# Kernel tuning notes

Measured on AMD Instinct MI355X. Metric: run time of the kernel, lower is better.

Reference implementation:

```python
import jax, jax.numpy as jnp
import numpy as np

N_NODES = 100000
N_EDGES = 1600000
IN_DIM = 128
HID2 = 128   # hidden_dim * 2
OUT_DIM = 1


def setup_inputs() -> dict:
    key = jax.random.key(0)
    ks = jax.random.split(key, 9)
    x = jax.random.normal(ks[0], (N_NODES, IN_DIM), dtype=jnp.float32)
    edge_index = jax.random.randint(ks[1], (2, N_EDGES), 0, N_NODES, dtype=jnp.int32)
    s_in = 1.0 / np.sqrt(IN_DIM)
    s_h = 1.0 / np.sqrt(HID2)
    W_conv = jax.random.normal(ks[2], (IN_DIM, HID2), dtype=jnp.float32) * s_in
    b_conv = jnp.zeros((HID2,), dtype=jnp.float32)
    W_proj = jax.random.normal(ks[3], (IN_DIM, HID2), dtype=jnp.float32) * s_in
    b_proj = jax.random.normal(ks[4], (HID2,), dtype=jnp.float32) * s_in
    W_out = jax.random.normal(ks[5], (HID2, OUT_DIM), dtype=jnp.float32) * s_h
    b_out = jax.random.normal(ks[6], (OUT_DIM,), dtype=jnp.float32) * s_h
    return {"x": x, "edge_index": edge_index, "W_conv": W_conv, "b_conv": b_conv,
            "W_proj": W_proj, "b_proj": b_proj, "W_out": W_out, "b_out": b_out}


def reference(x, edge_index, W_conv, b_conv, W_proj, b_proj, W_out, b_out):
    n = x.shape[0]
    loops = jnp.arange(n, dtype=edge_index.dtype)
    self_loops = jnp.stack([loops, loops])  # [2, N]
    # self loops added twice: once in forward() explicitly, once inside GCNConv (default)
    ei = jnp.concatenate([edge_index, self_loops, self_loops], axis=1)
    row, col = ei[0], ei[1]  # source -> destination
    # symmetric GCN normalization: deg computed over destinations
    deg = jax.ops.segment_sum(jnp.ones_like(row, dtype=x.dtype), col, num_segments=n)
    dinv = jnp.where(deg > 0, deg ** -0.5, 0.0)
    norm = dinv[row] * dinv[col]  # [E']
    xw = x @ W_conv  # [N, HID2]
    msgs = xw[row] * norm[:, None]  # [E', HID2] gather + scale
    conv = jax.ops.segment_sum(msgs, col, num_segments=n) + b_conv
    combined = jax.nn.relu(conv + x @ W_proj + b_proj)
    out = combined @ W_out + b_out  # [N, 1]
    return out.squeeze()
```

## Files before the change

### kernel.cpp

```cpp
#include <hip/hip_runtime.h>

#define N_NODES 100000
#define N_EDGES 1600000
#define DIM 128
#define NBIN 128
#define WINSZ 782
#define SLOT 64
#define CH 4096
#define NP1 ((N_EDGES + CH - 1) / CH)
#define SUBCAP 80
#define NGEMM ((N_NODES + 63) / 64)
#define SENT 0xFFFFFFFFu

typedef __attribute__((ext_vector_type(8))) short short8;
typedef __attribute__((ext_vector_type(4))) float f32x4;

__device__ inline unsigned short bf16u(float f) {
    unsigned u = __builtin_bit_cast(unsigned, f);
    return (unsigned short)((u + 0x7FFFu + ((u >> 16) & 1u)) >> 16);
}
__device__ inline unsigned pk_bf16(float a, float b) {
    return (unsigned)bf16u(a) | ((unsigned)bf16u(b) << 16);
}
__device__ inline float bf16_lo(unsigned v) { return __builtin_bit_cast(float, v << 16); }
__device__ inline float bf16_hi(unsigned v) { return __builtin_bit_cast(float, v & 0xFFFF0000u); }

__device__ inline unsigned pk_fp8x4(float a, float b, float c, float d) {
    int lo = __builtin_amdgcn_cvt_pk_fp8_f32(a, b, 0, false);
    int hi = __builtin_amdgcn_cvt_pk_fp8_f32(c, d, lo, true);
    return (unsigned)hi;
}
__device__ inline float fp8_b0(int v) { return __builtin_amdgcn_cvt_f32_fp8(v, 0); }
__device__ inline float fp8_b1(int v) { return __builtin_amdgcn_cvt_f32_fp8(v, 1); }


__launch_bounds__(256)
__global__ void k_prep(const float* __restrict__ Wc, const float* __restrict__ Wp,
                       const int* __restrict__ erow, const int* __restrict__ ecol,
                       int* __restrict__ cntT, unsigned* __restrict__ gbin,
                       unsigned short* __restrict__ WtG) {
    const int tid = threadIdx.x;
    if (blockIdx.x >= NP1) {
        int idx = (blockIdx.x - NP1) * 256 + tid;
        int n = idx >> 7, k = idx & 127;
        float v = (n < 128) ? Wc[k * 128 + n] : Wp[k * 128 + (n - 128)];
        int t = n >> 4, mm = n & 15;
        int q = k >> 5, qd = (k >> 3) & 3, j = k & 7;
        WtG[(((t * 4 + q) * 64 + qd * 16 + mm) << 3) + j] = bf16u(v);
        return;
    }
    __shared__ int lcnt[NBIN];
    const int blk = blockIdx.x;
    if (tid < NBIN) lcnt[tid] = 0;
    __syncthreads();
    const int e0 = blk * CH;
    const int e1 = (e0 + CH < N_EDGES) ? e0 + CH : N_EDGES;
    for (int e = e0 + tid; e < e1; e += 256) {
        int c = ecol[e];
        int bin = c / WINSZ;
        unsigned pay = (unsigned)erow[e] | ((unsigned)(c - bin * WINSZ) << 17);
        int r = atomicAdd(&lcnt[bin], 1);
        if (r < SUBCAP) gbin[((size_t)bin * NP1 + blk) * SUBCAP + r] = pay;
    }
    __syncthreads();
    if (tid < NBIN) {
        int v = lcnt[tid];
        cntT[blk * NBIN + tid] = (v < SUBCAP) ? v : SUBCAP;
    }
}

__launch_bounds__(256)
__global__ void k_bins(const int* __restrict__ cntT,
                       const unsigned* __restrict__ gbin,
                       int* __restrict__ srcb2,
                       int* __restrict__ cnt,
                       float* __restrict__ dinv) {
    __shared__ int lcnt[WINSZ];
    __shared__ int cl[NP1];
    const int tid = threadIdx.x;
    const int bin = blockIdx.x;
    const int lo  = bin * WINSZ;
    const int nw  = (lo + WINSZ < N_NODES) ? WINSZ : (N_NODES - lo);
    if (nw <= 0) return;
    for (int i = tid; i < WINSZ; i += 256) lcnt[i] = 0;
    for (int i = tid; i < NP1; i += 256) cl[i] = cntT[i * NBIN + bin];
    __syncthreads();

    const int wv = tid >> 6, ln = tid & 63;
    const int g = wv * 2 + (ln >> 5);
    const int lidx = ln & 31;
    const size_t binbase = (size_t)bin * NP1 * SUBCAP;

    int sg = g;
    int len = cl[sg];
    const unsigned* seg = gbin + binbase + (size_t)sg * SUBCAP;
    unsigned p0 = (lidx < len) ? seg[lidx] : SENT;
    unsigned p1 = (lidx + 32 < len) ? seg[lidx + 32] : SENT;

    while (sg < NP1) {
        const int nsg = sg + 8;
        int nlen = 0;
        const unsigned* nseg = seg;
        unsigned n0 = SENT, n1 = SENT;
        if (nsg < NP1) {
            nlen = cl[nsg];
            nseg = gbin + binbase + (size_t)nsg * SUBCAP;
            n0 = (lidx < nlen) ? nseg[lidx] : SENT;
            n1 = (lidx + 32 < nlen) ? nseg[lidx + 32] : SENT;
        }
        if (p0 != SENT) {
            int row = p0 & 0x1FFFF, c = p0 >> 17;
            int r = atomicAdd(&lcnt[c], 1);
            if (r < SLOT) srcb2[(lo + c) * SLOT + r] = row;
        }
        if (p1 != SENT) {
            int row = p1 & 0x1FFFF, c = p1 >> 17;
            int r = atomicAdd(&lcnt[c], 1);
            if (r < SLOT) srcb2[(lo + c) * SLOT + r] = row;
        }
        if (len > 64) {
            for (int i = lidx + 64; i < len; i += 32) {
                unsigned pay = seg[i];
                int row = pay & 0x1FFFF, c = pay >> 17;
                int r = atomicAdd(&lcnt[c], 1);
                if (r < SLOT) srcb2[(lo + c) * SLOT + r] = row;
            }
        }
        sg = nsg; len = nlen; seg = nseg; p0 = n0; p1 = n1;
    }
    __syncthreads();
    for (int i = tid; i < nw; i += 256) {
        int v = lcnt[i];
        cnt[lo + i]  = (v < SLOT) ? v : SLOT;
        dinv[lo + i] = rsqrtf((float)(v + 2));
    }
}

__global__ void k_gemm(const float* __restrict__ x,
                       const unsigned short* __restrict__ WtG,
                       const float* __restrict__ bc,
                       const float* __restrict__ bp,
                       unsigned* __restrict__ xwb8,
                       unsigned* __restrict__ accb) {
    __shared__ alignas(16) unsigned short wbuf[16384];

    const int tid   = threadIdx.x;
    const int node0 = blockIdx.x * 64;
    const int w     = tid >> 6;
    const int lane  = tid & 63;
    const int m     = lane & 15;
    const int quad  = lane >> 4;

    const uint4* gsrc = (const uint4*)WtG;
    uint4*       lbuf = (uint4*)wbuf;

    #pragma unroll
    for (int i = 0; i < 8; ++i) lbuf[i * 256 + tid] = gsrc[i * 256 + tid];

    const int  rowg  = node0 + w * 16 + m;
    const bool valid = rowg < N_NODES;
    const float* xrow = x + (size_t)rowg * DIM;

    short8 afr[4];
    #pragma unroll
    for (int q = 0; q < 4; q++) {
        float4 xa = make_float4(0.f, 0.f, 0.f, 0.f);
        float4 xb = make_float4(0.f, 0.f, 0.f, 0.f);
        if (valid) {
            xa = *(const float4*)(xrow + 32 * q + 8 * quad);
            xb = *(const float4*)(xrow + 32 * q + 8 * quad + 4);
        }
        uint4 pa;
        pa.x = pk_bf16(xa.x, xa.y); pa.y = pk_bf16(xa.z, xa.w);
        pa.z = pk_bf16(xb.x, xb.y); pa.w = pk_bf16(xb.z, xb.w);
        afr[q] = __builtin_bit_cast(short8, pa);
    }

    float bias[8];
    #pragma unroll
    for (int p = 0; p < 4; p++) {
        bias[2 * p]     = bc[32 * p + m]      + bp[32 * p + m];
        bias[2 * p + 1] = bc[32 * p + m + 16] + bp[32 * p + m + 16];
    }

    __syncthreads();

    f32x4 acc0[8];
    #pragma unroll
    for (int t = 0; t < 8; ++t) {
        f32x4 a = (f32x4){0.f, 0.f, 0.f, 0.f};
        #pragma unroll
        for (int q = 0; q < 4; ++q) {
            short8 bfrag = *(const short8*)(wbuf + (((t * 4 + q) * 64 + lane) << 3));
            a = __builtin_amdgcn_mfma_f32_16x16x32_bf16(afr[q], bfrag, a, 0, 0, 0);
        }
        acc0[t] = a;
    }

    #pragma unroll
    for (int r = 0; r < 4; ++r) {
        int node = node0 + w * 16 + quad * 4 + r;
        if (node < N_NODES) {
            uint2 xv;
            xv.x = pk_fp8x4(acc0[0][r], acc0[1][r], acc0[2][r], acc0[3][r]);
            xv.y = pk_fp8x4(acc0[4][r], acc0[5][r], acc0[6][r], acc0[7][r]);
            *(uint2*)(xwb8 + (size_t)node * 32 + m * 2) = xv;
        }
    }

    __syncthreads();

    #pragma unroll
    for (int i = 0; i < 8; ++i) lbuf[i * 256 + tid] = gsrc[2048 + i * 256 + tid];

    __syncthreads();

    f32x4 acc1[8];
    #pragma unroll
    for (int t = 0; t < 8; ++t) {
        f32x4 a = (f32x4){0.f, 0.f, 0.f, 0.f};
        #pragma unroll
        for (int q = 0; q < 4; ++q) {
            short8 bfrag = *(const short8*)(wbuf + (((t * 4 + q) * 64 + lane) << 3));
            a = __builtin_amdgcn_mfma_f32_16x16x32_bf16(afr[q], bfrag, a, 0, 0, 0);
        }
        acc1[t] = a;
    }

    #pragma unroll
    for (int r = 0; r < 4; ++r) {
        int node = node0 + w * 16 + quad * 4 + r;
        if (node < N_NODES) {
            uint4 pv;
            pv.x = pk_bf16(acc1[0][r] + bias[0], acc1[1][r] + bias[1]);
            pv.y = pk_bf16(acc1[2][r] + bias[2], acc1[3][r] + bias[3]);
            pv.z = pk_bf16(acc1[4][r] + bias[4], acc1[5][r] + bias[5]);
            pv.w = pk_bf16(acc1[6][r] + bias[6], acc1[7][r] + bias[7]);
            *(uint4*)(accb + (size_t)node * 64 + m * 4) = pv;
        }
    }
}

__launch_bounds__(256)
__global__ void k_gather_final(const int* __restrict__ srcb2,
                               const int* __restrict__ cnt,
                               const float* __restrict__ dinv,
                               const unsigned short* __restrict__ xw8,
                               const unsigned* __restrict__ accb,
                               const float* __restrict__ wout,
                               const float* __restrict__ bout,
                               float* __restrict__ out) {
    int t = blockIdx.x * 256 + threadIdx.x;
    int node = t >> 6;
    int lane = t & 63;
    if (node >= N_NODES) return;

    int c = cnt[node];
    const int* sp = srcb2 + node * SLOT;
    float ddst = dinv[node];

    unsigned av = accb[node * 64 + lane];
    float2 a;
    a.x = bf16_lo(av);
    a.y = bf16_hi(av);

    {
        int vs = xw8[(size_t)node * 64 + lane];
        float sl = 2.0f * ddst * ddst;
        a.x += fp8_b0(vs) * sl;
        a.y += fp8_b1(vs) * sl;
    }

    float2 b2 = make_float2(0.f, 0.f);
    int j = 0;
    for (; j + 8 <= c; j += 8) {
        int r0 = sp[j],     r1 = sp[j + 1], r2 = sp[j + 2], r3 = sp[j + 3];
        int r4 = sp[j + 4], r5 = sp[j + 5], r6 = sp[j + 6], r7 = sp[j + 7];
        int v0 = xw8[(size_t)r0 * 64 + lane], v1 = xw8[(size_t)r1 * 64 + lane];
        int v2 = xw8[(size_t)r2 * 64 + lane], v3 = xw8[(size_t)r3 * 64 + lane];
        int v4 = xw8[(size_t)r4 * 64 + lane], v5 = xw8[(size_t)r5 * 64 + lane];
        int v6 = xw8[(size_t)r6 * 64 + lane], v7 = xw8[(size_t)r7 * 64 + lane];
        float n0 = dinv[r0] * ddst, n1 = dinv[r1] * ddst;
        float n2 = dinv[r2] * ddst, n3 = dinv[r3] * ddst;
        float n4 = dinv[r4] * ddst, n5 = dinv[r5] * ddst;
        float n6 = dinv[r6] * ddst, n7 = dinv[r7] * ddst;
        a.x  += fp8_b0(v0) * n0 + fp8_b0(v1) * n1 + fp8_b0(v2) * n2 + fp8_b0(v3) * n3;
        a.y  += fp8_b1(v0) * n0 + fp8_b1(v1) * n1 + fp8_b1(v2) * n2 + fp8_b1(v3) * n3;
        b2.x += fp8_b0(v4) * n4 + fp8_b0(v5) * n5 + fp8_b0(v6) * n6 + fp8_b0(v7) * n7;
        b2.y += fp8_b1(v4) * n4 + fp8_b1(v5) * n5 + fp8_b1(v6) * n6 + fp8_b1(v7) * n7;
    }
    if (j < c) {
        const int mx = c - 1;
        int i1 = j + 1, i2 = j + 2, i3 = j + 3;
        int i4 = j + 4, i5 = j + 5, i6 = j + 6, i7 = j + 7;
        int r0 = sp[j];
        int r1 = sp[(i1 < mx) ? i1 : mx], r2 = sp[(i2 < mx) ? i2 : mx];
        int r3 = sp[(i3 < mx) ? i3 : mx], r4 = sp[(i4 < mx) ? i4 : mx];
        int r5 = sp[(i5 < mx) ? i5 : mx], r6 = sp[(i6 < mx) ? i6 : mx];
        int r7 = sp[(i7 < mx) ? i7 : mx];
        int v0 = xw8[(size_t)r0 * 64 + lane], v1 = xw8[(size_t)r1 * 64 + lane];
        int v2 = xw8[(size_t)r2 * 64 + lane], v3 = xw8[(size_t)r3 * 64 + lane];
        int v4 = xw8[(size_t)r4 * 64 + lane], v5 = xw8[(size_t)r5 * 64 + lane];
        int v6 = xw8[(size_t)r6 * 64 + lane], v7 = xw8[(size_t)r7 * 64 + lane];
        float n0 = dinv[r0] * ddst;
        float n1 = (i1 < c) ? dinv[r1] * ddst : 0.f;
        float n2 = (i2 < c) ? dinv[r2] * ddst : 0.f;
        float n3 = (i3 < c) ? dinv[r3] * ddst : 0.f;
        float n4 = (i4 < c) ? dinv[r4] * ddst : 0.f;
        float n5 = (i5 < c) ? dinv[r5] * ddst : 0.f;
        float n6 = (i6 < c) ? dinv[r6] * ddst : 0.f;
        float n7 = (i7 < c) ? dinv[r7] * ddst : 0.f;
        a.x  += fp8_b0(v0) * n0 + fp8_b0(v1) * n1 + fp8_b0(v2) * n2 + fp8_b0(v3) * n3;
        a.y  += fp8_b1(v0) * n0 + fp8_b1(v1) * n1 + fp8_b1(v2) * n2 + fp8_b1(v3) * n3;
        b2.x += fp8_b0(v4) * n4 + fp8_b0(v5) * n5 + fp8_b0(v6) * n6 + fp8_b0(v7) * n7;
        b2.y += fp8_b1(v4) * n4 + fp8_b1(v5) * n5 + fp8_b1(v6) * n6 + fp8_b1(v7) * n7;
    }
    a.x += b2.x;
    a.y += b2.y;

    int f0 = 32 * (lane & 3) + (lane >> 2);
    float w0 = wout[f0], w1 = wout[f0 + 16];
    float s = fmaxf(a.x, 0.f) * w0 + fmaxf(a.y, 0.f) * w1;
    #pragma unroll
    for (int off = 32; off > 0; off >>= 1) s += __shfl_down(s, off);
    if (lane == 0) out[node] = s + bout[0];
}

extern "C" void kernel_launch(void* const* d_in, const int* in_sizes, int n_in,
                              void* d_out, int out_size, void* d_ws, size_t ws_size,
                              hipStream_t stream) {
    const float* x      = (const float*)d_in[0];
    const int*   ei     = (const int*)  d_in[1];
    const float* W_conv = (const float*)d_in[2];
    const float* b_conv = (const float*)d_in[3];
    const float* W_proj = (const float*)d_in[4];
    const float* b_proj = (const float*)d_in[5];
    const float* W_out  = (const float*)d_in[6];
    const float* b_out  = (const float*)d_in[7];
    float* out = (float*)d_out;

    const int* e_row = ei;
    const int* e_col = ei + N_EDGES;

    char* p = (char*)d_ws;
    unsigned*       xwb8  = (unsigned*)p;       p += (size_t)N_NODES * 32 * 4;
    unsigned*       accb  = (unsigned*)p;       p += (size_t)N_NODES * 64 * 4;
    int*            srcb2 = (int*)p;            p += (size_t)N_NODES * SLOT * 4;
    unsigned*       gbin  = (unsigned*)p;       p += (size_t)NBIN * NP1 * SUBCAP * 4;
    int*            cntT  = (int*)p;            p += (size_t)NP1 * NBIN * 4;
    int*            cnt   = (int*)p;            p += (size_t)N_NODES * 4;
    float*          dinv  = (float*)p;          p += (size_t)N_NODES * 4;
    unsigned short* WtG   = (unsigned short*)p; p += 256 * 128 * 2;

    k_prep<<<NP1 + 128, 256, 0, stream>>>(W_conv, W_proj, e_row, e_col, cntT, gbin, WtG);
    k_gemm<<<NGEMM, 256, 0, stream>>>(x, WtG, b_conv, b_proj, xwb8, accb);
    k_bins<<<NBIN, 256, 0, stream>>>(cntT, gbin, srcb2, cnt, dinv);
    k_gather_final<<<(N_NODES * 64 + 255) / 256, 256, 0, stream>>>(
        srcb2, cnt, dinv, (const unsigned short*)xwb8, accb, W_out, b_out, out);
}
```

Before: 239.4 us.

## Pre-scale XW rows by source dinv in GEMM to drop per-edge dinv gathers

Moves the bins kernel ahead of the GEMM so dinv is ready, then folds the source-side normalization into the fp8 XW rows written by the GEMM. The gather kernel then just sums neighbor rows and applies the destination dinv once, which removes eight scattered dinv loads and multiplies per edge group. Neighbor indices are now read as int4 vectors and addresses use 32-bit shift/or. The cost is that k_gemm can no longer overlap with k_bins, and fp8 quantization now applies to values already scaled by dinv.

```diff
diff --git a/kernel.cpp b/kernel.cpp
--- a/kernel.cpp
+++ b/kernel.cpp
@@ -140,6 +140,7 @@
                        const unsigned short* __restrict__ WtG,
                        const float* __restrict__ bc,
                        const float* __restrict__ bp,
+                       const float* __restrict__ dinv,
                        unsigned* __restrict__ xwb8,
                        unsigned* __restrict__ accb) {
     __shared__ alignas(16) unsigned short wbuf[16384];
@@ -201,9 +202,12 @@
     for (int r = 0; r < 4; ++r) {
         int node = node0 + w * 16 + quad * 4 + r;
         if (node < N_NODES) {
+            float dv = dinv[node];
             uint2 xv;
-            xv.x = pk_fp8x4(acc0[0][r], acc0[1][r], acc0[2][r], acc0[3][r]);
-            xv.y = pk_fp8x4(acc0[4][r], acc0[5][r], acc0[6][r], acc0[7][r]);
+            xv.x = pk_fp8x4(acc0[0][r] * dv, acc0[1][r] * dv,
+                            acc0[2][r] * dv, acc0[3][r] * dv);
+            xv.y = pk_fp8x4(acc0[4][r] * dv, acc0[5][r] * dv,
+                            acc0[6][r] * dv, acc0[7][r] * dv);
             *(uint2*)(xwb8 + (size_t)node * 32 + m * 2) = xv;
         }
     }
@@ -252,42 +256,37 @@
                                float* __restrict__ out) {
     int t = blockIdx.x * 256 + threadIdx.x;
     int node = t >> 6;
-    int lane = t & 63;
+    unsigned lane = (unsigned)(t & 63);
     if (node >= N_NODES) return;
 
     int c = cnt[node];
     const int* sp = srcb2 + node * SLOT;
     float ddst = dinv[node];
 
-    unsigned av = accb[node * 64 + lane];
-    float2 a;
-    a.x = bf16_lo(av);
-    a.y = bf16_hi(av);
-
-    {
-        int vs = xw8[(size_t)node * 64 + lane];
-        float sl = 2.0f * ddst * ddst;
-        a.x += fp8_b0(vs) * sl;
-        a.y += fp8_b1(vs) * sl;
-    }
-
-    float2 b2 = make_float2(0.f, 0.f);
+    unsigned av = accb[(unsigned)node * 64u + lane];
+    float px = bf16_lo(av);
+    float py = bf16_hi(av);
+
+    int vs = xw8[((unsigned)node << 6) | lane];
+    float sx = 2.0f * fp8_b0(vs), sy = 2.0f * fp8_b1(vs);
+    float tx = 0.f, ty = 0.f;
+
     int j = 0;
     for (; j + 8 <= c; j += 8) {
-        int r0 = sp[j],     r1 = sp[j + 1], r2 = sp[j + 2], r3 = sp[j + 3];
-        int r4 = sp[j + 4], r5 = sp[j + 5], r6 = sp[j + 6], r7 = sp[j + 7];
-        int v0 = xw8[(size_t)r0 * 64 + lane], v1 = xw8[(size_t)r1 * 64 + lane];
-        int v2 = xw8[(size_t)r2 * 64 + lane], v3 = xw8[(size_t)r3 * 64 + lane];
-        int v4 = xw8[(size_t)r4 * 64 + lane], v5 = xw8[(size_t)r5 * 64 + lane];
-        int v6 = xw8[(size_t)r6 * 64 + lane], v7 = xw8[(size_t)r7 * 64 + lane];
-        float n0 = dinv[r0] * ddst, n1 = dinv[r1] * ddst;
-        float n2 = dinv[r2] * ddst, n3 = dinv[r3] * ddst;
-        float n4 = dinv[r4] * ddst, n5 = dinv[r5] * ddst;
-        float n6 = dinv[r6] * ddst, n7 = dinv[r7] * ddst;
-        a.x  += fp8_b0(v0) * n0 + fp8_b0(v1) * n1 + fp8_b0(v2) * n2 + fp8_b0(v3) * n3;
-        a.y  += fp8_b1(v0) * n0 + fp8_b1(v1) * n1 + fp8_b1(v2) * n2 + fp8_b1(v3) * n3;
-        b2.x += fp8_b0(v4) * n4 + fp8_b0(v5) * n5 + fp8_b0(v6) * n6 + fp8_b0(v7) * n7;
-        b2.y += fp8_b1(v4) * n4 + fp8_b1(v5) * n5 + fp8_b1(v6) * n6 + fp8_b1(v7) * n7;
+        int4 ra = *(const int4*)(sp + j);
+        int4 rb = *(const int4*)(sp + j + 4);
+        int v0 = xw8[((unsigned)ra.x << 6) | lane];
+        int v1 = xw8[((unsigned)ra.y << 6) | lane];
+        int v2 = xw8[((unsigned)ra.z << 6) | lane];
+        int v3 = xw8[((unsigned)ra.w << 6) | lane];
+        int v4 = xw8[((unsigned)rb.x << 6) | lane];
+        int v5 = xw8[((unsigned)rb.y << 6) | lane];
+        int v6 = xw8[((unsigned)rb.z << 6) | lane];
+        int v7 = xw8[((unsigned)rb.w << 6) | lane];
+        sx += fp8_b0(v0) + fp8_b0(v1) + fp8_b0(v2) + fp8_b0(v3);
+        sy += fp8_b1(v0) + fp8_b1(v1) + fp8_b1(v2) + fp8_b1(v3);
+        tx += fp8_b0(v4) + fp8_b0(v5) + fp8_b0(v6) + fp8_b0(v7);
+        ty += fp8_b1(v4) + fp8_b1(v5) + fp8_b1(v6) + fp8_b1(v7);
     }
     if (j < c) {
         const int mx = c - 1;
@@ -298,29 +297,29 @@
         int r3 = sp[(i3 < mx) ? i3 : mx], r4 = sp[(i4 < mx) ? i4 : mx];
         int r5 = sp[(i5 < mx) ? i5 : mx], r6 = sp[(i6 < mx) ? i6 : mx];
         int r7 = sp[(i7 < mx) ? i7 : mx];
-        int v0 = xw8[(size_t)r0 * 64 + lane], v1 = xw8[(size_t)r1 * 64 + lane];
-        int v2 = xw8[(size_t)r2 * 64 + lane], v3 = xw8[(size_t)r3 * 64 + lane];
-        int v4 = xw8[(size_t)r4 * 64 + lane], v5 = xw8[(size_t)r5 * 64 + lane];
-        int v6 = xw8[(size_t)r6 * 64 + lane], v7 = xw8[(size_t)r7 * 64 + lane];
-        float n0 = dinv[r0] * ddst;
-        float n1 = (i1 < c) ? dinv[r1] * ddst : 0.f;
-        float n2 = (i2 < c) ? dinv[r2] * ddst : 0.f;
-        float n3 = (i3 < c) ? dinv[r3] * ddst : 0.f;
-        float n4 = (i4 < c) ? dinv[r4] * ddst : 0.f;
-        float n5 = (i5 < c) ? dinv[r5] * ddst : 0.f;
-        float n6 = (i6 < c) ? dinv[r6] * ddst : 0.f;
-        float n7 = (i7 < c) ? dinv[r7] * ddst : 0.f;
-        a.x  += fp8_b0(v0) * n0 + fp8_b0(v1) * n1 + fp8_b0(v2) * n2 + fp8_b0(v3) * n3;
-        a.y  += fp8_b1(v0) * n0 + fp8_b1(v1) * n1 + fp8_b1(v2) * n2 + fp8_b1(v3) * n3;
-        b2.x += fp8_b0(v4) * n4 + fp8_b0(v5) * n5 + fp8_b0(v6) * n6 + fp8_b0(v7) * n7;
-        b2.y += fp8_b1(v4) * n4 + fp8_b1(v5) * n5 + fp8_b1(v6) * n6 + fp8_b1(v7) * n7;
-    }
-    a.x += b2.x;
-    a.y += b2.y;
+        int v0 = xw8[((unsigned)r0 << 6) | lane];
+        int v1 = xw8[((unsigned)r1 << 6) | lane];
+        int v2 = xw8[((unsigned)r2 << 6) | lane];
+        int v3 = xw8[((unsigned)r3 << 6) | lane];
+        int v4 = xw8[((unsigned)r4 << 6) | lane];
+        int v5 = xw8[((unsigned)r5 << 6) | lane];
+        int v6 = xw8[((unsigned)r6 << 6) | lane];
+        int v7 = xw8[((unsigned)r7 << 6) | lane];
+        v1 = (i1 < c) ? v1 : 0;  v2 = (i2 < c) ? v2 : 0;
+        v3 = (i3 < c) ? v3 : 0;  v4 = (i4 < c) ? v4 : 0;
+        v5 = (i5 < c) ? v5 : 0;  v6 = (i6 < c) ? v6 : 0;
+        v7 = (i7 < c) ? v7 : 0;
+        sx += fp8_b0(v0) + fp8_b0(v1) + fp8_b0(v2) + fp8_b0(v3);
+        sy += fp8_b1(v0) + fp8_b1(v1) + fp8_b1(v2) + fp8_b1(v3);
+        tx += fp8_b0(v4) + fp8_b0(v5) + fp8_b0(v6) + fp8_b0(v7);
+        ty += fp8_b1(v4) + fp8_b1(v5) + fp8_b1(v6) + fp8_b1(v7);
+    }
+    float ax = px + ddst * (sx + tx);
+    float ay = py + ddst * (sy + ty);
 
     int f0 = 32 * (lane & 3) + (lane >> 2);
     float w0 = wout[f0], w1 = wout[f0 + 16];
-    float s = fmaxf(a.x, 0.f) * w0 + fmaxf(a.y, 0.f) * w1;
+    float s = fmaxf(ax, 0.f) * w0 + fmaxf(ay, 0.f) * w1;
     #pragma unroll
     for (int off = 32; off > 0; off >>= 1) s += __shfl_down(s, off);
     if (lane == 0) out[node] = s + bout[0];
@@ -353,8 +352,8 @@
     unsigned short* WtG   = (unsigned short*)p; p += 256 * 128 * 2;
 
     k_prep<<<NP1 + 128, 256, 0, stream>>>(W_conv, W_proj, e_row, e_col, cntT, gbin, WtG);
-    k_gemm<<<NGEMM, 256, 0, stream>>>(x, WtG, b_conv, b_proj, xwb8, accb);
     k_bins<<<NBIN, 256, 0, stream>>>(cntT, gbin, srcb2, cnt, dinv);
+    k_gemm<<<NGEMM, 256, 0, stream>>>(x, WtG, b_conv, b_proj, dinv, xwb8, accb);
     k_gather_final<<<(N_NODES * 64 + 255) / 256, 256, 0, stream>>>(
         srcb2, cnt, dinv, (const unsigned short*)xwb8, accb, W_out, b_out, out);
 }
```

New measurement: 211.1 us. 1.13x faster.
